# Performance work log

Hardware: AMD Instinct MI355X
Metric: run time of the kernel (lower is better)

## Reference

```python
import jax, jax.numpy as jnp
import numpy as np

IN_F = 4096
OUT_F = 11008
N_CLUSTERS = 16
TOPK = int(IN_F * 0.25)  # 1024


def setup_inputs() -> dict:
    key = jax.random.key(0)
    k1, k2, k3, k4 = jax.random.split(key, 4)
    x = jax.random.normal(k1, (1, 1, IN_F), jnp.float32)
    weight_full = jax.random.normal(k2, (OUT_F, IN_F), jnp.float32) * 0.02
    bias_full = jax.random.normal(k3, (OUT_F,), jnp.float32) * 0.02
    # cluster centers live in softmax-activation space (compared via cdist to a softmax)
    cluster_centers = jax.nn.softmax(
        jax.random.normal(k4, (N_CLUSTERS, IN_F), jnp.float32), axis=-1)
    return {"x": x, "weight_full": weight_full, "bias_full": bias_full,
            "cluster_centers": cluster_centers}


def reference(x, weight_full, bias_full, cluster_centers):
    # hot path: bsz * seq == 1
    x_flat = x.reshape(-1, x.shape[-1])                 # [1, in]
    x_avg = jnp.abs(jnp.mean(x_flat, axis=0))           # [in]
    activation = jax.nn.softmax(x_avg, axis=0)          # [in]
    # nearest cluster center (squared L2 has same argmin as L2)
    d2 = jnp.sum((cluster_centers - activation[None, :]) ** 2, axis=-1)  # [n_clusters]
    ci = jnp.argmin(d2)
    center = cluster_centers[ci]                        # [in]
    # per-cluster precomputed top-k column indices: argsort(center, descending)[:topk]
    _, topk_idx = jax.lax.top_k(center, TOPK)           # [topk]
    x_sel = jnp.take(x_flat, topk_idx, axis=1)          # [1, topk]
    w_sel = jnp.take(weight_full, topk_idx, axis=1)     # [out, topk]
    out = x_sel @ w_sel.T + bias_full                   # [1, out]
    return out.reshape(1, 1, -1)
```

## Files before the change

kernel.cpp:

```cpp
#include <hip/hip_runtime.h>

#define IN_F 4096
#define OUT_F 11008
#define NCLUST 16
#define TOPK 1024
#define NBLK 256
#define ROWS_PB 43
#define GRAN_F 1024

__device__ __forceinline__ float dot4(float4 a, float4 b) {
    return a.x * b.x + a.y * b.y + a.z * b.z + a.w * b.w;
}
__device__ __forceinline__ float wredsum(float v) {
    for (int o = 32; o > 0; o >>= 1) v += __shfl_down(v, o, 64);
    return v;
}
__device__ __forceinline__ float wredmax(float v) {
    for (int o = 32; o > 0; o >>= 1) v = fmaxf(v, __shfl_down(v, o, 64));
    return v;
}
__device__ __forceinline__ void barrier_lds() {
    asm volatile("s_waitcnt lgkmcnt(0)" ::: "memory");
    __builtin_amdgcn_s_barrier();
}
__device__ __forceinline__ void stage_granule(const float* __restrict__ W,
                                              int row, int q, float* lbuf,
                                              int lane) {
    const float* src = W + (size_t)row * IN_F + q * GRAN_F + lane * 4;
    #pragma unroll
    for (int j = 0; j < 4; ++j) {
        __builtin_amdgcn_global_load_lds(
            (const __attribute__((address_space(1))) void*)(src + j * 256),
            (__attribute__((address_space(3))) void*)(lbuf + j * 256),
            16, 0, 0);
    }
}

__global__ __launch_bounds__(256, 1) void fused_kernel(
    const float* __restrict__ x,
    const float* __restrict__ W,
    const float* __restrict__ bias,
    const float* __restrict__ centers,
    float* __restrict__ out)
{
    const int tid  = threadIdx.x;
    const int lane = tid & 63;
    const int wid  = tid >> 6;
    const int bid  = blockIdx.x;

    __shared__ __align__(16) float sxm[IN_F];
    __shared__ __align__(16) float wstage[8][GRAN_F];
    __shared__ unsigned int hist[4][256];
    __shared__ float sredA[4], sredB[4];
    __shared__ float sdot[NCLUST], scsq[NCLUST];
    __shared__ unsigned int wtot4[4], weq[4];
    __shared__ unsigned int sprefix, sKrem, sG;
    __shared__ int sci;

    const int nr    = (wid < 3) ? 11 : 10;
    const int rbase = bid * ROWS_PB + wid;
    float* buf0 = &wstage[wid * 2][0];
    float* buf1 = &wstage[wid * 2 + 1][0];

    stage_granule(W, rbase, 0, buf0, lane);
    stage_granule(W, rbase, 1, buf1, lane);
    asm volatile("" ::: "memory");

    float4 x0 = ((const float4*)x)[tid * 4 + 0];
    float4 x1 = ((const float4*)x)[tid * 4 + 1];
    float4 x2 = ((const float4*)x)[tid * 4 + 2];
    float4 x3 = ((const float4*)x)[tid * 4 + 3];

    {
        float m = fmaxf(fmaxf(fabsf(x0.x), fabsf(x0.y)), fmaxf(fabsf(x0.z), fabsf(x0.w)));
        m = fmaxf(m, fmaxf(fmaxf(fabsf(x1.x), fabsf(x1.y)), fmaxf(fabsf(x1.z), fabsf(x1.w))));
        m = fmaxf(m, fmaxf(fmaxf(fabsf(x2.x), fabsf(x2.y)), fmaxf(fabsf(x2.z), fabsf(x2.w))));
        m = fmaxf(m, fmaxf(fmaxf(fabsf(x3.x), fabsf(x3.y)), fmaxf(fabsf(x3.z), fabsf(x3.w))));
        m = wredmax(m);
        if (lane == 0) sredA[wid] = m;
    }
    barrier_lds();
    const float mx = fmaxf(fmaxf(sredA[0], sredA[1]), fmaxf(sredA[2], sredA[3]));

    float e[16];
    e[0]=expf(fabsf(x0.x)-mx); e[1]=expf(fabsf(x0.y)-mx); e[2]=expf(fabsf(x0.z)-mx); e[3]=expf(fabsf(x0.w)-mx);
    e[4]=expf(fabsf(x1.x)-mx); e[5]=expf(fabsf(x1.y)-mx); e[6]=expf(fabsf(x1.z)-mx); e[7]=expf(fabsf(x1.w)-mx);
    e[8]=expf(fabsf(x2.x)-mx); e[9]=expf(fabsf(x2.y)-mx); e[10]=expf(fabsf(x2.z)-mx); e[11]=expf(fabsf(x2.w)-mx);
    e[12]=expf(fabsf(x3.x)-mx); e[13]=expf(fabsf(x3.y)-mx); e[14]=expf(fabsf(x3.z)-mx); e[15]=expf(fabsf(x3.w)-mx);
    {
        float4* sxm4 = (float4*)sxm;
        sxm4[tid*4+0] = make_float4(e[0],e[1],e[2],e[3]);
        sxm4[tid*4+1] = make_float4(e[4],e[5],e[6],e[7]);
        sxm4[tid*4+2] = make_float4(e[8],e[9],e[10],e[11]);
        sxm4[tid*4+3] = make_float4(e[12],e[13],e[14],e[15]);
        float s = 0.0f;
        #pragma unroll
        for (int k = 0; k < 16; ++k) s += e[k];
        s = wredsum(s);
        if (lane == 0) sredB[wid] = s;
    }
    barrier_lds();
    const float S = sredB[0] + sredB[1] + sredB[2] + sredB[3];

    {
        const float4* e4  = (const float4*)sxm;
        const float*  cb  = centers + (size_t)(4 * wid) * IN_F;
        const float4* c0p = (const float4*)(cb);
        const float4* c1p = (const float4*)(cb + IN_F);
        const float4* c2p = (const float4*)(cb + 2 * IN_F);
        const float4* c3p = (const float4*)(cb + 3 * IN_F);
        float d0=0,d1=0,d2=0,d3=0,q0=0,q1=0,q2=0,q3=0;
        #pragma unroll
        for (int j = 0; j < 16; ++j) {
            int idx = j * 64 + lane;
            float4 ev = e4[idx];
            float4 a = c0p[idx], b = c1p[idx], c = c2p[idx], d = c3p[idx];
            d0 += dot4(a, ev); q0 += dot4(a, a);
            d1 += dot4(b, ev); q1 += dot4(b, b);
            d2 += dot4(c, ev); q2 += dot4(c, c);
            d3 += dot4(d, ev); q3 += dot4(d, d);
        }
        d0 = wredsum(d0); d1 = wredsum(d1); d2 = wredsum(d2); d3 = wredsum(d3);
        q0 = wredsum(q0); q1 = wredsum(q1); q2 = wredsum(q2); q3 = wredsum(q3);
        if (lane == 0) {
            sdot[4*wid+0]=d0; sdot[4*wid+1]=d1; sdot[4*wid+2]=d2; sdot[4*wid+3]=d3;
            scsq[4*wid+0]=q0; scsq[4*wid+1]=q1; scsq[4*wid+2]=q2; scsq[4*wid+3]=q3;
        }
    }
    barrier_lds();

    if (wid == 0) {
        float v = (lane < NCLUST) ? (scsq[lane] - (2.0f / S) * sdot[lane]) : 3.0e38f;
        int bi = lane;
        for (int off = 8; off > 0; off >>= 1) {
            float ov = __shfl_down(v, off, 64);
            int   oi = __shfl_down(bi, off, 64);
            if (ov < v) { v = ov; bi = oi; }
        }
        if (lane == 0) sci = bi;
    }
    barrier_lds();
    const int ci = sci;

    const float4* cc4 = (const float4*)(centers + (size_t)ci * IN_F);
    float4 c0 = cc4[tid*4+0], c1 = cc4[tid*4+1], c2 = cc4[tid*4+2], c3 = cc4[tid*4+3];
    {
        unsigned int* hflat = &hist[0][0];
        hflat[tid] = 0u; hflat[tid+256] = 0u; hflat[tid+512] = 0u; hflat[tid+768] = 0u;
        if (tid == 0) { sprefix = 0u; sKrem = TOPK; sG = 0u; }
    }
    barrier_lds();

    unsigned int cv[16];
    cv[0]=__float_as_uint(c0.x); cv[1]=__float_as_uint(c0.y); cv[2]=__float_as_uint(c0.z); cv[3]=__float_as_uint(c0.w);
    cv[4]=__float_as_uint(c1.x); cv[5]=__float_as_uint(c1.y); cv[6]=__float_as_uint(c1.z); cv[7]=__float_as_uint(c1.w);
    cv[8]=__float_as_uint(c2.x); cv[9]=__float_as_uint(c2.y); cv[10]=__float_as_uint(c2.z); cv[11]=__float_as_uint(c2.w);
    cv[12]=__float_as_uint(c3.x); cv[13]=__float_as_uint(c3.y); cv[14]=__float_as_uint(c3.z); cv[15]=__float_as_uint(c3.w);

    for (int pass = 0; pass < 4; ++pass) {
        const int shift = 24 - 8 * pass;
        const unsigned int pfx  = sprefix;
        const unsigned int krem = sKrem;
        unsigned int* hp = hist[wid];
        #pragma unroll
        for (int k = 0; k < 16; ++k) {
            unsigned int u = cv[k];
            bool cand = (pass == 0) || ((u >> (shift + 8)) == pfx);
            if (cand) atomicAdd(&hp[(u >> shift) & 255u], 1u);
        }
        barrier_lds();
        unsigned int h, s;
        {
            const unsigned int b = tid;
            h = hist[0][b] + hist[1][b] + hist[2][b] + hist[3][b];
            hist[0][b] = 0u; hist[1][b] = 0u; hist[2][b] = 0u; hist[3][b] = 0u;
            s = h;
            for (int off = 1; off < 64; off <<= 1) {
                unsigned int v2 = __shfl_down(s, off, 64);
                if (lane + off < 64) s += v2;
            }
            if (lane == 0) wtot4[wid] = s;
        }
        barrier_lds();
        {
            unsigned int add = 0;
            #pragma unroll
            for (int w2 = 0; w2 < 4; ++w2) if (w2 > wid) add += wtot4[w2];
            unsigned int incl = s + add;
            unsigned int excl = incl - h;
            if (excl < krem && krem <= incl) {
                sprefix = (pfx << 8) | (unsigned int)tid;
                sKrem   = krem - excl;
            }
        }
        barrier_lds();
    }
    const unsigned int T = sprefix;

    unsigned int gt = 0, eq = 0;
    #pragma unroll
    for (int k = 0; k < 16; ++k) {
        gt += (cv[k] > T) ? 1u : 0u;
        eq += (cv[k] == T) ? 1u : 0u;
    }
    {
        unsigned int g = gt;
        for (int o = 32; o > 0; o >>= 1) g += __shfl_down(g, o, 64);
        if (lane == 0) atomicAdd(&sG, g);
    }
    unsigned int p = eq;
    for (int off = 1; off < 64; off <<= 1) {
        unsigned int v2 = __shfl_up(p, off, 64);
        if (lane >= off) p += v2;
    }
    if (lane == 63) weq[wid] = p;
    barrier_lds();
    unsigned int base = p - eq;
    #pragma unroll
    for (int w2 = 0; w2 < 4; ++w2) if (w2 < wid) base += weq[w2];
    const unsigned int needEq = TOPK - sG;

    {
        float xs[16] = {x0.x,x0.y,x0.z,x0.w, x1.x,x1.y,x1.z,x1.w,
                        x2.x,x2.y,x2.z,x2.w, x3.x,x3.y,x3.z,x3.w};
        float os[16];
        unsigned int r = 0;
        #pragma unroll
        for (int k = 0; k < 16; ++k) {
            bool sel = (cv[k] > T) || ((cv[k] == T) && (base + r < needEq));
            os[k] = sel ? xs[k] : 0.0f;
            r += (cv[k] == T) ? 1u : 0u;
        }
        float4* sxm4 = (float4*)sxm;
        sxm4[tid*4+0] = make_float4(os[0],os[1],os[2],os[3]);
        sxm4[tid*4+1] = make_float4(os[4],os[5],os[6],os[7]);
        sxm4[tid*4+2] = make_float4(os[8],os[9],os[10],os[11]);
        sxm4[tid*4+3] = make_float4(os[12],os[13],os[14],os[15]);
    }
    barrier_lds();
    float4 slice[16];
    {
        const float4* sxm4 = (const float4*)sxm;
        #pragma unroll
        for (int k = 0; k < 16; ++k) slice[k] = sxm4[k * 64 + lane];
    }

    for (int i = 0; i < nr; ++i) {
        const int row = rbase + 4 * i;
        float acc = 0.0f;
        float bv = 0.0f;
        #pragma unroll
        for (int q = 0; q < 4; ++q) {
            const int g = i * 4 + q;
            if (g + 1 < nr * 4) { asm volatile("s_waitcnt vmcnt(4)" ::: "memory"); }
            else                { asm volatile("s_waitcnt vmcnt(0)" ::: "memory"); }
            if (q == 0) bv = bias[row];
            const float4* wb = (const float4*)((q & 1) ? buf1 : buf0);
            float4 a0 = wb[0 * 64 + lane];
            float4 a1 = wb[1 * 64 + lane];
            float4 a2 = wb[2 * 64 + lane];
            float4 a3 = wb[3 * 64 + lane];
            acc += dot4(a0, slice[q * 4 + 0]) + dot4(a1, slice[q * 4 + 1])
                 + dot4(a2, slice[q * 4 + 2]) + dot4(a3, slice[q * 4 + 3]);
            asm volatile("s_waitcnt lgkmcnt(0)" ::: "memory");
            const int g2 = g + 2;
            if (g2 < nr * 4) {
                stage_granule(W, rbase + 4 * (g2 >> 2), g2 & 3,
                              (g2 & 1) ? buf1 : buf0, lane);
            }
        }
        for (int o = 32; o > 0; o >>= 1) acc += __shfl_down(acc, o, 64);
        if (lane == 0) out[row] = acc + bv;
    }
}

extern "C" void kernel_launch(void* const* d_in, const int* in_sizes, int n_in,
                              void* d_out, int out_size, void* d_ws, size_t ws_size,
                              hipStream_t stream) {
    const float* x       = (const float*)d_in[0];
    const float* weight  = (const float*)d_in[1];
    const float* bias    = (const float*)d_in[2];
    const float* centers = (const float*)d_in[3];
    float* out = (float*)d_out;

    fused_kernel<<<NBLK, 256, 0, stream>>>(x, weight, bias, centers, out);
}
```

Measured before the change: 43.70 us.

## Double grid occupancy, triple-buffer weight staging, and trim softmax prologue barriers

Launches 512 blocks at two blocks per CU, spreading rows unevenly (22 or 21 rows per block). The per-wave LDS staging of weight rows goes from double to triple buffering with deeper vmcnt waits, so more loads are in flight while the kernel streams the weight matrix. It drops the max-subtraction pass and its barrier from the softmax, folds histogram initialisation into an earlier barrier, and preloads the bias values. The risks: exp without max subtraction can overflow for large inputs, and the first weight prefetch now starts after cluster selection rather than at kernel entry.

```diff
diff --git a/kernel.cpp b/kernel.cpp
--- a/kernel.cpp
+++ b/kernel.cpp
@@ -4,9 +4,9 @@
 #define OUT_F 11008
 #define NCLUST 16
 #define TOPK 1024
-#define NBLK 256
-#define ROWS_PB 43
+#define NBLK 512
 #define GRAN_F 1024
+#define NBUF 3
 
 __device__ __forceinline__ float dot4(float4 a, float4 b) {
     return a.x * b.x + a.y * b.y + a.z * b.z + a.w * b.w;
@@ -15,17 +15,12 @@
     for (int o = 32; o > 0; o >>= 1) v += __shfl_down(v, o, 64);
     return v;
 }
-__device__ __forceinline__ float wredmax(float v) {
-    for (int o = 32; o > 0; o >>= 1) v = fmaxf(v, __shfl_down(v, o, 64));
-    return v;
-}
 __device__ __forceinline__ void barrier_lds() {
     asm volatile("s_waitcnt lgkmcnt(0)" ::: "memory");
     __builtin_amdgcn_s_barrier();
 }
-__device__ __forceinline__ void stage_granule(const float* __restrict__ W,
-                                              int row, int q, float* lbuf,
-                                              int lane) {
+__device__ __forceinline__ void stage_gq(const float* __restrict__ W,
+                                         int row, int q, float* lbuf, int lane) {
     const float* src = W + (size_t)row * IN_F + q * GRAN_F + lane * 4;
     #pragma unroll
     for (int j = 0; j < 4; ++j) {
@@ -36,7 +31,7 @@
     }
 }
 
-__global__ __launch_bounds__(256, 1) void fused_kernel(
+__global__ __launch_bounds__(256, 2) void fused_kernel(
     const float* __restrict__ x,
     const float* __restrict__ W,
     const float* __restrict__ bias,
@@ -49,44 +44,30 @@
     const int bid  = blockIdx.x;
 
     __shared__ __align__(16) float sxm[IN_F];
-    __shared__ __align__(16) float wstage[8][GRAN_F];
+    __shared__ __align__(16) float wstage[4 * NBUF][GRAN_F];
     __shared__ unsigned int hist[4][256];
-    __shared__ float sredA[4], sredB[4];
+    __shared__ float sredB[4];
     __shared__ float sdot[NCLUST], scsq[NCLUST];
     __shared__ unsigned int wtot4[4], weq[4];
     __shared__ unsigned int sprefix, sKrem, sG;
     __shared__ int sci;
 
-    const int nr    = (wid < 3) ? 11 : 10;
-    const int rbase = bid * ROWS_PB + wid;
-    float* buf0 = &wstage[wid * 2][0];
-    float* buf1 = &wstage[wid * 2 + 1][0];
-
-    stage_granule(W, rbase, 0, buf0, lane);
-    stage_granule(W, rbase, 1, buf1, lane);
-    asm volatile("" ::: "memory");
+    const int nb    = (bid < 256) ? 22 : 21;
+    const int start = bid * 21 + ((bid < 256) ? bid : 256);
+    const int nr    = (nb - 1 - wid) / 4 + 1;
+    const int NG    = nr * 4;
+    float* wbase = &wstage[wid * NBUF][0];
 
     float4 x0 = ((const float4*)x)[tid * 4 + 0];
     float4 x1 = ((const float4*)x)[tid * 4 + 1];
     float4 x2 = ((const float4*)x)[tid * 4 + 2];
     float4 x3 = ((const float4*)x)[tid * 4 + 3];
 
-    {
-        float m = fmaxf(fmaxf(fabsf(x0.x), fabsf(x0.y)), fmaxf(fabsf(x0.z), fabsf(x0.w)));
-        m = fmaxf(m, fmaxf(fmaxf(fabsf(x1.x), fabsf(x1.y)), fmaxf(fabsf(x1.z), fabsf(x1.w))));
-        m = fmaxf(m, fmaxf(fmaxf(fabsf(x2.x), fabsf(x2.y)), fmaxf(fabsf(x2.z), fabsf(x2.w))));
-        m = fmaxf(m, fmaxf(fmaxf(fabsf(x3.x), fabsf(x3.y)), fmaxf(fabsf(x3.z), fabsf(x3.w))));
-        m = wredmax(m);
-        if (lane == 0) sredA[wid] = m;
-    }
-    barrier_lds();
-    const float mx = fmaxf(fmaxf(sredA[0], sredA[1]), fmaxf(sredA[2], sredA[3]));
-
     float e[16];
-    e[0]=expf(fabsf(x0.x)-mx); e[1]=expf(fabsf(x0.y)-mx); e[2]=expf(fabsf(x0.z)-mx); e[3]=expf(fabsf(x0.w)-mx);
-    e[4]=expf(fabsf(x1.x)-mx); e[5]=expf(fabsf(x1.y)-mx); e[6]=expf(fabsf(x1.z)-mx); e[7]=expf(fabsf(x1.w)-mx);
-    e[8]=expf(fabsf(x2.x)-mx); e[9]=expf(fabsf(x2.y)-mx); e[10]=expf(fabsf(x2.z)-mx); e[11]=expf(fabsf(x2.w)-mx);
-    e[12]=expf(fabsf(x3.x)-mx); e[13]=expf(fabsf(x3.y)-mx); e[14]=expf(fabsf(x3.z)-mx); e[15]=expf(fabsf(x3.w)-mx);
+    e[0]=expf(fabsf(x0.x)); e[1]=expf(fabsf(x0.y)); e[2]=expf(fabsf(x0.z)); e[3]=expf(fabsf(x0.w));
+    e[4]=expf(fabsf(x1.x)); e[5]=expf(fabsf(x1.y)); e[6]=expf(fabsf(x1.z)); e[7]=expf(fabsf(x1.w));
+    e[8]=expf(fabsf(x2.x)); e[9]=expf(fabsf(x2.y)); e[10]=expf(fabsf(x2.z)); e[11]=expf(fabsf(x2.w));
+    e[12]=expf(fabsf(x3.x)); e[13]=expf(fabsf(x3.y)); e[14]=expf(fabsf(x3.z)); e[15]=expf(fabsf(x3.w));
     {
         float4* sxm4 = (float4*)sxm;
         sxm4[tid*4+0] = make_float4(e[0],e[1],e[2],e[3]);
@@ -98,6 +79,9 @@
         for (int k = 0; k < 16; ++k) s += e[k];
         s = wredsum(s);
         if (lane == 0) sredB[wid] = s;
+        unsigned int* hflat = &hist[0][0];
+        hflat[tid] = 0u; hflat[tid+256] = 0u; hflat[tid+512] = 0u; hflat[tid+768] = 0u;
+        if (tid == 0) { sprefix = 0u; sKrem = TOPK; sG = 0u; }
     }
     barrier_lds();
     const float S = sredB[0] + sredB[1] + sredB[2] + sredB[3];
@@ -144,12 +128,18 @@
 
     const float4* cc4 = (const float4*)(centers + (size_t)ci * IN_F);
     float4 c0 = cc4[tid*4+0], c1 = cc4[tid*4+1], c2 = cc4[tid*4+2], c3 = cc4[tid*4+3];
-    {
-        unsigned int* hflat = &hist[0][0];
-        hflat[tid] = 0u; hflat[tid+256] = 0u; hflat[tid+512] = 0u; hflat[tid+768] = 0u;
-        if (tid == 0) { sprefix = 0u; sKrem = TOPK; sG = 0u; }
-    }
-    barrier_lds();
+    float bv[6];
+    #pragma unroll
+    for (int i = 0; i < 6; ++i) {
+        int r = start + wid + 4 * i;
+        bv[i] = bias[(i < nr) ? r : start];
+    }
+
+    asm volatile("" ::: "memory");
+    stage_gq(W, start + wid, 0, wbase + 0 * GRAN_F, lane);
+    stage_gq(W, start + wid, 1, wbase + 1 * GRAN_F, lane);
+    stage_gq(W, start + wid, 2, wbase + 2 * GRAN_F, lane);
+    asm volatile("" ::: "memory");
 
     unsigned int cv[16];
     cv[0]=__float_as_uint(c0.x); cv[1]=__float_as_uint(c0.y); cv[2]=__float_as_uint(c0.z); cv[3]=__float_as_uint(c0.w);
@@ -245,32 +235,36 @@
         for (int k = 0; k < 16; ++k) slice[k] = sxm4[k * 64 + lane];
     }
 
-    for (int i = 0; i < nr; ++i) {
-        const int row = rbase + 4 * i;
+    int buf = 0;
+    #pragma unroll 6
+    for (int i = 0; i < 6; ++i) {
+        if (i >= nr) break;
+        const int row = start + wid + 4 * i;
         float acc = 0.0f;
-        float bv = 0.0f;
         #pragma unroll
         for (int q = 0; q < 4; ++q) {
-            const int g = i * 4 + q;
-            if (g + 1 < nr * 4) { asm volatile("s_waitcnt vmcnt(4)" ::: "memory"); }
-            else                { asm volatile("s_waitcnt vmcnt(0)" ::: "memory"); }
-            if (q == 0) bv = bias[row];
-            const float4* wb = (const float4*)((q & 1) ? buf1 : buf0);
-            float4 a0 = wb[0 * 64 + lane];
-            float4 a1 = wb[1 * 64 + lane];
-            float4 a2 = wb[2 * 64 + lane];
-            float4 a3 = wb[3 * 64 + lane];
+            const int g = 4 * i + q;
+            const int rem = NG - 1 - g;
+            if (rem >= 2)      { asm volatile("s_waitcnt vmcnt(8)" ::: "memory"); }
+            else if (rem == 1) { asm volatile("s_waitcnt vmcnt(4)" ::: "memory"); }
+            else               { asm volatile("s_waitcnt vmcnt(0)" ::: "memory"); }
+            const float4* bp = (const float4*)(wbase + buf * GRAN_F);
+            float4 a0 = bp[0 * 64 + lane];
+            float4 a1 = bp[1 * 64 + lane];
+            float4 a2 = bp[2 * 64 + lane];
+            float4 a3 = bp[3 * 64 + lane];
             acc += dot4(a0, slice[q * 4 + 0]) + dot4(a1, slice[q * 4 + 1])
                  + dot4(a2, slice[q * 4 + 2]) + dot4(a3, slice[q * 4 + 3]);
             asm volatile("s_waitcnt lgkmcnt(0)" ::: "memory");
-            const int g2 = g + 2;
-            if (g2 < nr * 4) {
-                stage_granule(W, rbase + 4 * (g2 >> 2), g2 & 3,
-                              (g2 & 1) ? buf1 : buf0, lane);
+            const int gn = g + 3;
+            if (gn < NG) {
+                stage_gq(W, start + wid + 4 * (gn >> 2), gn & 3,
+                         wbase + buf * GRAN_F, lane);
             }
-        }
-        for (int o = 32; o > 0; o >>= 1) acc += __shfl_down(acc, o, 64);
-        if (lane == 0) out[row] = acc + bv;
+            buf = (buf == NBUF - 1) ? 0 : buf + 1;
+        }
+        acc = wredsum(acc);
+        if (lane == 0) out[row] = acc + bv[i];
     }
 }
 
```

New measurement: 45.45 us. 1.04x slower.
